# Performance work log

Measured on AMD Instinct MI355X. Metric: run time of the kernel, lower is better.

The kernel has to match this reference:

```python
import jax, jax.numpy as jnp
import numpy as np

D_MODEL = 1024
NUM_HEADS = 16
DEPTH = D_MODEL // NUM_HEADS
TEMPERATURE = 1.0
B, S = 2, 2048


def setup_inputs() -> dict:
    key = jax.random.key(0)
    ks = jax.random.split(key, 13)
    s = 1.0 / np.sqrt(D_MODEL)
    return {
        "query": jax.random.normal(ks[0], (B, S, D_MODEL), jnp.float32),
        "key": jax.random.normal(ks[1], (B, S, D_MODEL), jnp.float32),
        "value": jax.random.normal(ks[2], (B, S, D_MODEL), jnp.float32),
        "temporal_bias": jax.random.normal(ks[3], (B, S), jnp.float32),
        "wq": jax.random.normal(ks[4], (D_MODEL, D_MODEL), jnp.float32) * s,
        "bq": jnp.zeros((D_MODEL,), jnp.float32),
        "wk": jax.random.normal(ks[5], (D_MODEL, D_MODEL), jnp.float32) * s,
        "bk": jnp.zeros((D_MODEL,), jnp.float32),
        "wv": jax.random.normal(ks[6], (D_MODEL, D_MODEL), jnp.float32) * s,
        "bv": jnp.zeros((D_MODEL,), jnp.float32),
        "wo": jax.random.normal(ks[7], (D_MODEL, D_MODEL), jnp.float32) * s,
        "bo": jnp.zeros((D_MODEL,), jnp.float32),
    }


def _split_heads(x):
    b, s, _ = x.shape
    return x.reshape(b, s, NUM_HEADS, DEPTH).transpose(0, 2, 1, 3)  # [B,H,S,depth]


def reference(query, key, value, temporal_bias, wq, bq, wk, bk, wv, bv, wo, bo):
    q = _split_heads(query @ wq + bq)
    k = _split_heads(key @ wk + bk)
    v = _split_heads(value @ wv + bv)
    scale = jnp.sqrt(jnp.asarray(DEPTH, q.dtype)) * TEMPERATURE
    logits = jnp.einsum("bhqd,bhkd->bhqk", q, k) / scale
    logits = logits + temporal_bias[:, None, None, :]  # per-key additive bias
    attn = jax.nn.softmax(logits, axis=-1)
    out = jnp.einsum("bhqk,bhkd->bhqd", attn, v)
    out = out.transpose(0, 2, 1, 3).reshape(query.shape[0], -1, D_MODEL)
    return out @ wo + bo
```

## Files before the change

### kernel.cpp

```cpp
#include <hip/hip_runtime.h>
#include <hip/hip_fp16.h>


typedef _Float16 f16;
typedef _Float16 f16x8 __attribute__((ext_vector_type(8)));
typedef float f32x4 __attribute__((ext_vector_type(4)));
typedef float f32x16 __attribute__((ext_vector_type(16)));
typedef unsigned int u32;

#define LOG2E 1.4426950408889634f

static constexpr int Bb   = 2;
static constexpr int Ss   = 2048;
static constexpr int Hh   = 16;
static constexpr int Dh   = 64;
static constexpr int Dm   = 1024;
static constexpr int Mrows = Bb * Ss;

__device__ __forceinline__ float fast_exp2(float x) {
#if __has_builtin(__builtin_amdgcn_exp2f)
    return __builtin_amdgcn_exp2f(x);
#else
    return exp2f(x);
#endif
}

__device__ __forceinline__ u32 pk2(float a, float b) {
    auto h = __builtin_amdgcn_cvt_pkrtz(a, b);
    return __builtin_bit_cast(u32, h);
}

__global__ void k_cvt(const float* __restrict__ s0, const float* __restrict__ s1,
                      const float* __restrict__ s2,
                      f16* __restrict__ d0, f16* __restrict__ d1, f16* __restrict__ d2) {
    const float* src; f16* dst;
    if (blockIdx.z == 0)      { src = s0; dst = d0; }
    else if (blockIdx.z == 1) { src = s1; dst = d1; }
    else                      { src = s2; dst = d2; }
    int i = (blockIdx.x * 256 + threadIdx.x) * 8;
    float4 a = *(const float4*)(src + i);
    float4 b = *(const float4*)(src + i + 4);
    f16x8 h;
    h[0] = (f16)a.x; h[1] = (f16)a.y; h[2] = (f16)a.z; h[3] = (f16)a.w;
    h[4] = (f16)b.x; h[5] = (f16)b.y; h[6] = (f16)b.z; h[7] = (f16)b.w;
    *(f16x8*)(dst + i) = h;
}

__global__ void k_transpose(const float* __restrict__ w0, const float* __restrict__ w1,
                            const float* __restrict__ w2, const float* __restrict__ w3,
                            f16* __restrict__ t0, f16* __restrict__ t1,
                            f16* __restrict__ t2, f16* __restrict__ t3) {
    __shared__ float tile[64][65];
    const float* W; f16* T;
    switch (blockIdx.z) {
        case 0:  W = w0; T = t0; break;
        case 1:  W = w1; T = t1; break;
        case 2:  W = w2; T = t2; break;
        default: W = w3; T = t3; break;
    }
    const int t  = threadIdx.x;
    const int rr = t >> 6;
    const int cc = t & 63;
    const int k0 = blockIdx.x * 64;
    const int n0 = blockIdx.y * 64;
#pragma unroll
    for (int i = 0; i < 16; ++i) {
        int r = i * 4 + rr;
        tile[r][cc] = W[(size_t)(k0 + r) * Dm + n0 + cc];
    }
    __syncthreads();
#pragma unroll
    for (int i = 0; i < 16; ++i) {
        int rn = i * 4 + rr;
        T[(size_t)(n0 + rn) * Dm + k0 + cc] = (f16)tile[cc][rn];
    }
}

__global__ __launch_bounds__(256) void k_transpose_v(const f16* __restrict__ vh,
                                                     f16* __restrict__ vt) {
    __shared__ f16 tile[64][72];
    const int tid = threadIdx.x;
    const int bh  = blockIdx.y;
    const int sb  = blockIdx.x;
    const f16* src = vh + ((size_t)bh * Ss + sb * 64) * Dh;
#pragma unroll
    for (int pp = 0; pp < 2; ++pp) {
        int r  = pp * 32 + (tid >> 3);
        int ch = tid & 7;
        *(f16x8*)&tile[r][ch * 8] = *(const f16x8*)&src[r * Dh + ch * 8];
    }
    __syncthreads();
#pragma unroll
    for (int pp = 0; pp < 2; ++pp) {
        int d  = pp * 32 + (tid >> 3);
        int s0 = (tid & 7) * 8;
        f16x8 o;
#pragma unroll
        for (int j = 0; j < 8; ++j) o[j] = tile[s0 + j][d];
        *(f16x8*)&vt[((size_t)bh * Dh + d) * Ss + sb * 64 + s0] = o;
    }
}

__device__ __forceinline__ void gload16(const void* g, void* l) {
    __builtin_amdgcn_global_load_lds(
        (const __attribute__((address_space(1))) unsigned int*)g,
        (__attribute__((address_space(3))) unsigned int*)l, 16, 0, 0);
}

__global__ __launch_bounds__(256) void k_gemm(
        const f16* __restrict__ Xb, const f16* __restrict__ Wtb,
        const float* __restrict__ b0, const float* __restrict__ b1,
        const float* __restrict__ b2,
        f16* __restrict__ outHb, float* __restrict__ outF, float scale0) {
    const int z = blockIdx.z;
    const f16* X  = Xb  + (size_t)z * ((size_t)Mrows * Dm);
    const f16* Wt = Wtb + (size_t)z * ((size_t)Dm * Dm);
    const float* bias = (z == 0) ? b0 : (z == 1 ? b1 : b2);
    const float scale = (z == 0) ? scale0 : 1.0f;

    __shared__ __align__(16) f16 As[128 * 32];
    __shared__ __align__(16) f16 Bs[128 * 32];
    const int tid = threadIdx.x;
    const int l   = tid & 63;
    const int w   = tid >> 6;
    const int g   = l >> 4;
    const int c16 = l & 15;
    const int tM = blockIdx.x * 128;
    const int tN = blockIdx.y * 128;
    const int wm = w >> 1, wn = w & 1;

    f32x4 acc[4][4] = {};

    auto stage = [&](int kt) {
#pragma unroll
        for (int cc = 0; cc < 2; ++cc) {
            int c   = w * 2 + cc;
            int row = c * 16 + (l >> 2);
            int ob  = (l & 3) * 16;
            gload16((const char*)X  + (size_t)(tM + row) * 2048 + (size_t)kt * 64 + ob,
                    (char*)As + c * 1024 + l * 16);
            gload16((const char*)Wt + (size_t)(tN + row) * 2048 + (size_t)kt * 64 + ob,
                    (char*)Bs + c * 1024 + l * 16);
        }
    };

    stage(0);
    for (int kt = 0; kt < 32; ++kt) {
        __syncthreads();
        f16x8 af[4], bf[4];
#pragma unroll
        for (int fr = 0; fr < 4; ++fr)
            af[fr] = *(const f16x8*)&As[(wm * 64 + fr * 16 + c16) * 32 + g * 8];
#pragma unroll
        for (int fn = 0; fn < 4; ++fn)
            bf[fn] = *(const f16x8*)&Bs[(wn * 64 + fn * 16 + c16) * 32 + g * 8];
#pragma unroll
        for (int fr = 0; fr < 4; ++fr)
#pragma unroll
            for (int fn = 0; fn < 4; ++fn)
                acc[fr][fn] = __builtin_amdgcn_mfma_f32_16x16x32_f16(
                                  af[fr], bf[fn], acc[fr][fn], 0, 0, 0);
        __syncthreads();
        if (kt + 1 < 32) stage(kt + 1);
    }

    f16* outH = outHb ? outHb + (size_t)z * ((size_t)Mrows * Dm) : nullptr;
#pragma unroll
    for (int fr = 0; fr < 4; ++fr) {
#pragma unroll
        for (int fn = 0; fn < 4; ++fn) {
            int col = tN + wn * 64 + fn * 16 + c16;
            float bv = bias[col];
#pragma unroll
            for (int r = 0; r < 4; ++r) {
                int m = tM + wm * 64 + fr * 16 + g * 4 + r;
                float v = (acc[fr][fn][r] + bv) * scale;
                if (outF) {
                    outF[(size_t)m * Dm + col] = v;
                } else {
                    int b = m >> 11, s = m & 2047;
                    int h = col >> 6, d = col & 63;
                    outH[(((size_t)(b * Hh + h)) * Ss + s) * Dh + d] = (f16)v;
                }
            }
        }
    }
}

__global__ __launch_bounds__(256) void k_attn(
        const f16* __restrict__ Qh, const f16* __restrict__ Kh, const f16* __restrict__ Vt,
        const float* __restrict__ tb, f16* __restrict__ outX) {
    __shared__ __align__(16) f16 KV[2][2][64 * 72];
    __shared__ float TBL[2][64];

    const int tid  = threadIdx.x;
    const int lane = tid & 63, w = tid >> 6;
    const int l31  = lane & 31;
    const int h2   = lane >> 5;
    const int bh = blockIdx.y;
    const int b  = bh >> 4;
    const int h  = bh & 15;
    const int qb = blockIdx.x;

    const f16* Qbase = Qh + ((size_t)bh * Ss + qb * 128) * Dh;
    const f16* Kbase = Kh + (size_t)bh * Ss * Dh;
    const f16* Vtg   = Vt + (size_t)bh * Dh * Ss;
    const float* tbb = tb + (size_t)b * Ss;

    f16x8 qf[4];
    {
        const f16* qp = &Qbase[(w * 32 + l31) * Dh + h2 * 8];
#pragma unroll
        for (int s = 0; s < 4; ++s) qf[s] = *(const f16x8*)&qp[s * 16];
    }

    f32x16 o0 = {}, o1 = {};
    float m_run = -1e30f, l_run = 0.f;

    const int sr = tid >> 3;
    const int sc = (tid & 7) * 8;
    f16x8 kr0, kr1, vr0, vr1; float tr = 0.f;

    auto issue = [&](int kb) {
        kr0 = *(const f16x8*)&Kbase[((size_t)kb * 64 + sr) * Dh + sc];
        kr1 = *(const f16x8*)&Kbase[((size_t)kb * 64 + sr + 32) * Dh + sc];
        vr0 = *(const f16x8*)&Vtg[(size_t)sr * Ss + kb * 64 + sc];
        vr1 = *(const f16x8*)&Vtg[(size_t)(sr + 32) * Ss + kb * 64 + sc];
        if (tid < 64) tr = tbb[kb * 64 + tid];
    };
    auto commit = [&](int buf) {
        *(f16x8*)&KV[buf][0][sr * 72 + sc]        = kr0;
        *(f16x8*)&KV[buf][0][(sr + 32) * 72 + sc] = kr1;
        *(f16x8*)&KV[buf][1][sr * 72 + sc]        = vr0;
        *(f16x8*)&KV[buf][1][(sr + 32) * 72 + sc] = vr1;
        if (tid < 64) TBL[buf][tid] = tr;
    };

    issue(0);
    commit(0);
    __syncthreads();

    for (int kb = 0; kb < 32; ++kb) {
        const int buf = kb & 1;
        if (kb < 31) issue(kb + 1);

        const f16* Kl = &KV[buf][0][0];
        const f16* Vl = &KV[buf][1][0];
        const float* tl = TBL[buf];

        f32x16 s0 = {}, s1 = {};
#pragma unroll
        for (int s = 0; s < 4; ++s) {
            f16x8 a0 = *(const f16x8*)&Kl[l31 * 72 + s * 16 + h2 * 8];
            f16x8 a1 = *(const f16x8*)&Kl[(l31 + 32) * 72 + s * 16 + h2 * 8];
            s0 = __builtin_amdgcn_mfma_f32_32x32x16_f16(a0, qf[s], s0, 0, 0, 0);
            s1 = __builtin_amdgcn_mfma_f32_32x32x16_f16(a1, qf[s], s1, 0, 0, 0);
        }
#pragma unroll
        for (int t = 0; t < 4; ++t) {
            f32x4 bb0 = *(const f32x4*)&tl[t * 8 + h2 * 4];
            f32x4 bb1 = *(const f32x4*)&tl[32 + t * 8 + h2 * 4];
#pragma unroll
            for (int c = 0; c < 4; ++c) {
                s0[t * 4 + c] = fmaf(bb0[c], LOG2E, s0[t * 4 + c]);
                s1[t * 4 + c] = fmaf(bb1[c], LOG2E, s1[t * 4 + c]);
            }
        }

        float mx = s0[0];
#pragma unroll
        for (int r = 1; r < 16; ++r) mx = fmaxf(mx, s0[r]);
#pragma unroll
        for (int r = 0; r < 16; ++r) mx = fmaxf(mx, s1[r]);
        mx = fmaxf(mx, __shfl_xor(mx, 32));
        float m_new = fmaxf(m_run, mx);
        float rs = fast_exp2(m_run - m_new);
        m_run = m_new;

        float p0[16], p1[16];
        float sum = 0.f;
#pragma unroll
        for (int r = 0; r < 16; ++r) { p0[r] = fast_exp2(s0[r] - m_new); sum += p0[r]; }
#pragma unroll
        for (int r = 0; r < 16; ++r) { p1[r] = fast_exp2(s1[r] - m_new); sum += p1[r]; }
        sum += __shfl_xor(sum, 32);
        l_run = l_run * rs + sum;
#pragma unroll
        for (int r = 0; r < 16; ++r) { o0[r] *= rs; o1[r] *= rs; }

        u32 own[8][2], oth[8][2];
#pragma unroll
        for (int m = 0; m < 4; ++m) {
            own[m][0] = pk2(p0[4 * m + 0], p0[4 * m + 1]);
            own[m][1] = pk2(p0[4 * m + 2], p0[4 * m + 3]);
            own[m + 4][0] = pk2(p1[4 * m + 0], p1[4 * m + 1]);
            own[m + 4][1] = pk2(p1[4 * m + 2], p1[4 * m + 3]);
        }
#pragma unroll
        for (int m = 0; m < 8; ++m) {
            oth[m][0] = (u32)__shfl_xor((int)own[m][0], 32);
            oth[m][1] = (u32)__shfl_xor((int)own[m][1], 32);
        }

#pragma unroll
        for (int s = 0; s < 4; ++s) {
            const int m = 2 * s + h2;
            union { u32 u[4]; f16x8 v; } pf;
            if (h2 == 0) { pf.u[0] = own[m][0]; pf.u[1] = own[m][1];
                           pf.u[2] = oth[m][0]; pf.u[3] = oth[m][1]; }
            else         { pf.u[0] = oth[m][0]; pf.u[1] = oth[m][1];
                           pf.u[2] = own[m][0]; pf.u[3] = own[m][1]; }
            f16x8 va0 = *(const f16x8*)&Vl[l31 * 72 + s * 16 + h2 * 8];
            f16x8 va1 = *(const f16x8*)&Vl[(l31 + 32) * 72 + s * 16 + h2 * 8];
            o0 = __builtin_amdgcn_mfma_f32_32x32x16_f16(va0, pf.v, o0, 0, 0, 0);
            o1 = __builtin_amdgcn_mfma_f32_32x32x16_f16(va1, pf.v, o1, 0, 0, 0);
        }

        if (kb < 31) {
            commit((kb + 1) & 1);
            __syncthreads();
        }
    }

    __syncthreads();
    f16* Os = &KV[0][0][0];
    const float inv = 1.f / l_run;
    const int qloc = w * 32 + l31;
#pragma unroll
    for (int dm = 0; dm < 2; ++dm) {
#pragma unroll
        for (int t = 0; t < 4; ++t) {
            float e0 = (dm ? o1[4 * t + 0] : o0[4 * t + 0]) * inv;
            float e1 = (dm ? o1[4 * t + 1] : o0[4 * t + 1]) * inv;
            float e2 = (dm ? o1[4 * t + 2] : o0[4 * t + 2]) * inv;
            float e3 = (dm ? o1[4 * t + 3] : o0[4 * t + 3]) * inv;
            uint2 pkd = { pk2(e0, e1), pk2(e2, e3) };
            int d0 = dm * 32 + t * 8 + h2 * 4;
            *(uint2*)&Os[qloc * 72 + d0] = pkd;
        }
    }
    __syncthreads();
    const size_t obase = ((size_t)b * Ss + qb * 128) * Dm + h * 64;
#pragma unroll
    for (int i = 0; i < 2; ++i) {
        int c   = tid + i * 256;
        int row = c >> 2;
        int col = (c & 3) * 16;
        f16x8 va = *(const f16x8*)&Os[row * 72 + col];
        f16x8 vb = *(const f16x8*)&Os[row * 72 + col + 8];
        *(f16x8*)&outX[obase + (size_t)row * Dm + col]     = va;
        *(f16x8*)&outX[obase + (size_t)row * Dm + col + 8] = vb;
    }
}

extern "C" void kernel_launch(void* const* d_in, const int* in_sizes, int n_in,
                              void* d_out, int out_size, void* d_ws, size_t ws_size,
                              hipStream_t stream) {
    const float* q  = (const float*)d_in[0];
    const float* k  = (const float*)d_in[1];
    const float* v  = (const float*)d_in[2];
    const float* tb = (const float*)d_in[3];
    const float* wq = (const float*)d_in[4];
    const float* bq = (const float*)d_in[5];
    const float* wk = (const float*)d_in[6];
    const float* bk = (const float*)d_in[7];
    const float* wv = (const float*)d_in[8];
    const float* bv = (const float*)d_in[9];
    const float* wo = (const float*)d_in[10];
    const float* bo = (const float*)d_in[11];

    f16* ws = (f16*)d_ws;
    const size_t NX = (size_t)Mrows * Dm;
    const size_t NW = (size_t)Dm * Dm;
    f16* xq  = ws;
    f16* xk  = ws + NX;
    f16* xv  = ws + 2 * NX;
    f16* qh  = ws + 3 * NX;
    f16* kh  = ws + 4 * NX;
    f16* vh  = ws + 5 * NX;
    f16* wqt = ws + 6 * NX;
    f16* wkt = wqt + NW;
    f16* wvt = wkt + NW;
    f16* wot = wvt + NW;
    f16* ax  = xq;
    f16* vt  = xv;

    k_cvt<<<dim3(2048, 1, 3), 256, 0, stream>>>(q, k, v, xq, xk, xv);
    k_transpose<<<dim3(16, 16, 4), 256, 0, stream>>>(wq, wk, wv, wo, wqt, wkt, wvt, wot);
    k_gemm<<<dim3(32, 8, 3), 256, 0, stream>>>(xq, wqt, bq, bk, bv, qh, nullptr,
                                               0.125f * LOG2E);
    k_transpose_v<<<dim3(32, 32), 256, 0, stream>>>(vh, vt);
    k_attn<<<dim3(16, 32), 256, 0, stream>>>(qh, kh, vt, tb, ax);
    k_gemm<<<dim3(32, 8, 1), 256, 0, stream>>>(ax, wot, bo, bo, bo, nullptr,
                                               (float*)d_out, 1.0f);
}
```

Baseline: 254.0 us.

## Double GEMM K-tile depth and add lazy softmax rescaling with tree reductions

```diff
diff --git a/kernel.cpp b/kernel.cpp
--- a/kernel.cpp
+++ b/kernel.cpp
@@ -118,8 +118,8 @@
     const float* bias = (z == 0) ? b0 : (z == 1 ? b1 : b2);
     const float scale = (z == 0) ? scale0 : 1.0f;
 
-    __shared__ __align__(16) f16 As[128 * 32];
-    __shared__ __align__(16) f16 Bs[128 * 32];
+    __shared__ __align__(16) f16 As[128 * 64];
+    __shared__ __align__(16) f16 Bs[128 * 64];
     const int tid = threadIdx.x;
     const int l   = tid & 63;
     const int w   = tid >> 6;
@@ -131,37 +131,43 @@
 
     f32x4 acc[4][4] = {};
 
+    const int srow = tid >> 3;
+    const int sob  = (tid & 7) * 16;
     auto stage = [&](int kt) {
 #pragma unroll
-        for (int cc = 0; cc < 2; ++cc) {
-            int c   = w * 2 + cc;
-            int row = c * 16 + (l >> 2);
-            int ob  = (l & 3) * 16;
-            gload16((const char*)X  + (size_t)(tM + row) * 2048 + (size_t)kt * 64 + ob,
-                    (char*)As + c * 1024 + l * 16);
-            gload16((const char*)Wt + (size_t)(tN + row) * 2048 + (size_t)kt * 64 + ob,
-                    (char*)Bs + c * 1024 + l * 16);
+        for (int c = 0; c < 4; ++c) {
+            int row = c * 32 + srow;
+            gload16((const char*)X  + (size_t)(tM + row) * 2048 + (size_t)kt * 128 + sob,
+                    (char*)As + c * 4096 + tid * 16);
+            gload16((const char*)Wt + (size_t)(tN + row) * 2048 + (size_t)kt * 128 + sob,
+                    (char*)Bs + c * 4096 + tid * 16);
         }
     };
 
     stage(0);
-    for (int kt = 0; kt < 32; ++kt) {
+    for (int kt = 0; kt < 16; ++kt) {
         __syncthreads();
-        f16x8 af[4], bf[4];
+        f16x8 af[4][2], bf[4][2];
 #pragma unroll
         for (int fr = 0; fr < 4; ++fr)
-            af[fr] = *(const f16x8*)&As[(wm * 64 + fr * 16 + c16) * 32 + g * 8];
+#pragma unroll
+            for (int ks = 0; ks < 2; ++ks)
+                af[fr][ks] = *(const f16x8*)&As[(wm * 64 + fr * 16 + c16) * 64 + ks * 32 + g * 8];
 #pragma unroll
         for (int fn = 0; fn < 4; ++fn)
-            bf[fn] = *(const f16x8*)&Bs[(wn * 64 + fn * 16 + c16) * 32 + g * 8];
-#pragma unroll
-        for (int fr = 0; fr < 4; ++fr)
-#pragma unroll
-            for (int fn = 0; fn < 4; ++fn)
-                acc[fr][fn] = __builtin_amdgcn_mfma_f32_16x16x32_f16(
-                                  af[fr], bf[fn], acc[fr][fn], 0, 0, 0);
+#pragma unroll
+            for (int ks = 0; ks < 2; ++ks)
+                bf[fn][ks] = *(const f16x8*)&Bs[(wn * 64 + fn * 16 + c16) * 64 + ks * 32 + g * 8];
+#pragma unroll
+        for (int ks = 0; ks < 2; ++ks)
+#pragma unroll
+            for (int fr = 0; fr < 4; ++fr)
+#pragma unroll
+                for (int fn = 0; fn < 4; ++fn)
+                    acc[fr][fn] = __builtin_amdgcn_mfma_f32_16x16x32_f16(
+                                      af[fr][ks], bf[fn][ks], acc[fr][fn], 0, 0, 0);
         __syncthreads();
-        if (kt + 1 < 32) stage(kt + 1);
+        if (kt + 1 < 16) stage(kt + 1);
     }
 
     f16* outH = outHb ? outHb + (size_t)z * ((size_t)Mrows * Dm) : nullptr;
@@ -267,26 +273,36 @@
             }
         }
 
-        float mx = s0[0];
-#pragma unroll
-        for (int r = 1; r < 16; ++r) mx = fmaxf(mx, s0[r]);
-#pragma unroll
-        for (int r = 0; r < 16; ++r) mx = fmaxf(mx, s1[r]);
-        mx = fmaxf(mx, __shfl_xor(mx, 32));
-        float m_new = fmaxf(m_run, mx);
-        float rs = fast_exp2(m_run - m_new);
-        m_run = m_new;
+        float a8[8];
+#pragma unroll
+        for (int i = 0; i < 8; ++i)
+            a8[i] = fmaxf(fmaxf(s0[i], s0[i + 8]), fmaxf(s1[i], s1[i + 8]));
+        float pmax = fmaxf(fmaxf(fmaxf(a8[0], a8[1]), fmaxf(a8[2], a8[3])),
+                           fmaxf(fmaxf(a8[4], a8[5]), fmaxf(a8[6], a8[7])));
+        pmax = fmaxf(pmax, __shfl_xor(pmax, 32));
+
+        if (!__all(pmax - m_run <= 8.f)) {
+            float m_new = fmaxf(m_run, pmax);
+            float rs = fast_exp2(m_run - m_new);
+            m_run = m_new;
+            l_run *= rs;
+#pragma unroll
+            for (int r = 0; r < 16; ++r) { o0[r] *= rs; o1[r] *= rs; }
+        }
 
         float p0[16], p1[16];
-        float sum = 0.f;
-#pragma unroll
-        for (int r = 0; r < 16; ++r) { p0[r] = fast_exp2(s0[r] - m_new); sum += p0[r]; }
-#pragma unroll
-        for (int r = 0; r < 16; ++r) { p1[r] = fast_exp2(s1[r] - m_new); sum += p1[r]; }
+#pragma unroll
+        for (int r = 0; r < 16; ++r) p0[r] = fast_exp2(s0[r] - m_run);
+#pragma unroll
+        for (int r = 0; r < 16; ++r) p1[r] = fast_exp2(s1[r] - m_run);
+        float t8[8];
+#pragma unroll
+        for (int i = 0; i < 8; ++i)
+            t8[i] = (p0[i] + p0[i + 8]) + (p1[i] + p1[i + 8]);
+        float sum = ((t8[0] + t8[1]) + (t8[2] + t8[3])) +
+                    ((t8[4] + t8[5]) + (t8[6] + t8[7]));
         sum += __shfl_xor(sum, 32);
-        l_run = l_run * rs + sum;
-#pragma unroll
-        for (int r = 0; r < 16; ++r) { o0[r] *= rs; o1[r] *= rs; }
+        l_run += sum;
 
         u32 own[8][2], oth[8][2];
 #pragma unroll
```

After: 255.6 us. Within noise of the previous version (+0.6%).
